# Kernel tuning notes

Measured on AMD Instinct MI355X. Metric: run time of the kernel, lower is better.

Reference implementation:

```python
import jax, jax.numpy as jnp
import numpy as np

UNITS = 1024
FEATURES = 16
OUT_STEPS = 24
LEAK = 0.001
MASK_VALUE = -1.0


def _plstm_step(h, c, x, kernel, rec_kernel, bias, period, phase, ratio_on):
    # Keras LSTMCell: gates ordered i, f, g, o
    z = x @ kernel + h @ rec_kernel + bias  # [B, 4U]
    i, f, g, o = jnp.split(z, 4, axis=-1)
    i = jax.nn.sigmoid(i)
    f = jax.nn.sigmoid(f)
    o = jax.nn.sigmoid(o)
    new_c = f * c + i * jnp.tanh(g)
    new_h = o * jnp.tanh(new_c)
    # phased time gate: time is the first feature channel
    t = x[:, :1]  # [B,1]
    cr = jnp.mod(t - phase, period) / period  # [B,U], floor-mod like tf %
    k_up = 2.0 * cr / ratio_on
    k = jnp.where(cr < ratio_on, 2.0 - k_up, LEAK * cr)
    k = jnp.where(cr < 0.5 * ratio_on, k_up, k)
    h_out = k * new_h + (1.0 - k) * h
    c_out = k * new_c + (1.0 - k) * c
    return h_out, c_out


def _dense_stack(h, w1, b1, w2, b2, w3, b3, wo, bo):
    h = jnp.tanh(h @ w1 + b1)
    h = jnp.tanh(h @ w2 + b2)
    h = jnp.tanh(h @ w3 + b3)
    return h @ wo + bo


def setup_inputs() -> dict:
    key = jax.random.key(0)
    ks = jax.random.split(key, 16)
    U, F = UNITS, FEATURES
    s = 1.0 / np.sqrt(U)
    x = jax.random.normal(ks[0], (256, 512, F), dtype=jnp.float32)
    kernel = jax.random.normal(ks[1], (F, 4 * U), dtype=jnp.float32) * (1.0 / np.sqrt(F))
    rec_kernel = jax.random.normal(ks[2], (U, 4 * U), dtype=jnp.float32) * s
    bias = jnp.zeros((4 * U,), dtype=jnp.float32)
    log_p = jax.random.uniform(ks[3], (U,), minval=jnp.log(1.0), maxval=jnp.log(100.0))
    period = jnp.exp(log_p).astype(jnp.float32)
    phase = (jax.random.uniform(ks[4], (U,)) * period).astype(jnp.float32)
    ratio_on = jnp.full((U,), 0.1, dtype=jnp.float32)
    w1 = jax.random.normal(ks[5], (U, U // 4), dtype=jnp.float32) * s
    b1 = jnp.zeros((U // 4,), dtype=jnp.float32)
    w2 = jax.random.normal(ks[6], (U // 4, U // 8), dtype=jnp.float32) * (1.0 / np.sqrt(U // 4))
    b2 = jnp.zeros((U // 8,), dtype=jnp.float32)
    w3 = jax.random.normal(ks[7], (U // 8, U // 16), dtype=jnp.float32) * (1.0 / np.sqrt(U // 8))
    b3 = jnp.zeros((U // 16,), dtype=jnp.float32)
    wo = jax.random.normal(ks[8], (U // 16, F), dtype=jnp.float32) * (1.0 / np.sqrt(U // 16))
    bo = jnp.zeros((F,), dtype=jnp.float32)
    return dict(x=x, kernel=kernel, rec_kernel=rec_kernel, bias=bias,
                period=period, phase=phase, ratio_on=ratio_on,
                w1=w1, b1=b1, w2=w2, b2=b2, w3=w3, b3=b3, wo=wo, bo=bo)


def reference(x, kernel, rec_kernel, bias, period, phase, ratio_on,
              w1, b1, w2, b2, w3, b3, wo, bo):
    B = x.shape[0]
    U = rec_kernel.shape[0]
    h0 = jnp.zeros((B, U), dtype=x.dtype)
    c0 = jnp.zeros((B, U), dtype=x.dtype)

    # warmup RNN over the input sequence (Masking(-1.0): skip all -1 steps)
    def warm_step(carry, xt):
        h, c = carry
        mask = jnp.any(xt != MASK_VALUE, axis=-1, keepdims=True)  # [B,1]
        hn, cn = _plstm_step(h, c, xt, kernel, rec_kernel, bias, period, phase, ratio_on)
        h = jnp.where(mask, hn, h)
        c = jnp.where(mask, cn, c)
        return (h, c), None

    (h, c), _ = jax.lax.scan(warm_step, (h0, c0), jnp.swapaxes(x, 0, 1))

    pred0 = _dense_stack(h, w1, b1, w2, b2, w3, b3, wo, bo)  # [B,F]

    def ar_step(carry, _):
        h, c, p = carry
        h, c = _plstm_step(h, c, p, kernel, rec_kernel, bias, period, phase, ratio_on)
        p = _dense_stack(h, w1, b1, w2, b2, w3, b3, wo, bo)
        return (h, c, p), p

    _, preds = jax.lax.scan(ar_step, (h, c, pred0), None, length=OUT_STEPS - 1)
    preds = jnp.concatenate([pred0[None], preds], axis=0)  # [S,B,F]
    return jnp.transpose(preds, (1, 0, 2))  # [B, out_steps, F]
```

## Files before the change

### kernel.cpp

```cpp
#include <hip/hip_runtime.h>
#include <hip/hip_bf16.h>

#define UNITS 1024
#define FEAT  16
#define TSTEPS 512
#define OUTSTEPS 24
#define BATCH 256
#define KTOT  1088
#define NROWS 4096

#define MPB   32
#define RPB   128
#define BSB   2320
#define HST2_OFF 74240
#define SMEM_BYTES 83968

#define NGBAR   96
#define CTR_TOT ((TSTEPS * 8 + NGBAR) * 16)

typedef __bf16 bf16x8 __attribute__((ext_vector_type(8)));
typedef float  f32x4  __attribute__((ext_vector_type(4)));

__device__ __forceinline__ float sigmoidf_(float x) { return 1.f / (1.f + __expf(-x)); }
__device__ __forceinline__ float tanhf_(float x)    { return 1.f - 2.f / (__expf(2.f * x) + 1.f); }

__global__ __launch_bounds__(256) void prep_weights(const float* __restrict__ kern,
                                                    const float* __restrict__ rec,
                                                    __bf16* __restrict__ Wcat) {
    __shared__ __align__(16) __bf16 tile[64][72];
    int r0 = blockIdx.x * 64;
    int k0 = blockIdx.y * 64;
    int t  = threadIdx.x;
    int c_off = t & 63;
    int k_grp = t >> 6;
    int g = c_off >> 4, ui = c_off & 15;
    int u0 = r0 >> 2;
    int c  = g * 1024 + u0 + ui;
    int rl = 4 * ui + g;
    for (int i = 0; i < 16; i++) {
        int k = k0 + k_grp * 16 + i;
        float v = 0.f;
        if (k < 16)        v = kern[(size_t)k * NROWS + c];
        else if (k < 1040) v = rec[(size_t)(k - 16) * NROWS + c];
        tile[rl][k_grp * 16 + i] = (__bf16)v;
    }
    __syncthreads();
    int rl2 = t >> 2, ch = t & 3;
    bf16x8* dst = (bf16x8*)(Wcat + (size_t)(r0 + rl2) * KTOT + k0 + ch * 16);
    const bf16x8* src = (const bf16x8*)&tile[rl2][ch * 16];
    dst[0] = src[0];
    dst[1] = src[1];
}

__global__ __launch_bounds__(256) void prep_state(const float* __restrict__ x,
                                                  __bf16* __restrict__ Ab0,
                                                  __bf16* __restrict__ Ab1,
                                                  float* __restrict__ hT,
                                                  unsigned int* __restrict__ ctr) {
    int tid = blockIdx.x * 256 + threadIdx.x;
    int np  = gridDim.x * 256;
    for (int i = tid; i < BATCH * UNITS; i += np) hT[i] = 0.f;
    const int AB = BATCH * KTOT;
    for (int i = tid; i < 2 * AB; i += np) {
        int which = (i < AB) ? 0 : 1;
        int p = i - which * AB;
        int col = p % KTOT;
        int m   = p / KTOT;
        __bf16 v = (__bf16)0.f;
        if (which == 0 && col < FEAT) v = (__bf16)x[(size_t)m * TSTEPS * FEAT + col];
        if (which == 0) Ab0[p] = v; else Ab1[p] = v;
    }
    for (int i = tid; i < CTR_TOT; i += np) ctr[i] = 0u;
}

__global__ __launch_bounds__(256) void prep_tv(const float* __restrict__ x,
                                               float* __restrict__ tvx,
                                               unsigned char* __restrict__ kflag,
                                               __bf16* __restrict__ xbf) {
    int m = blockIdx.x;
    for (int t = threadIdx.x; t < TSTEPS; t += 256) {
        const float* row = x + ((size_t)m * TSTEPS + t) * FEAT;
        f32x4 v0 = *(const f32x4*)row;
        f32x4 v1 = *(const f32x4*)(row + 4);
        f32x4 v2 = *(const f32x4*)(row + 8);
        f32x4 v3 = *(const f32x4*)(row + 12);
        bool keep = true;
#pragma unroll
        for (int i = 0; i < 4; ++i)
            keep = keep && (v0[i] == -1.f) && (v1[i] == -1.f) &&
                   (v2[i] == -1.f) && (v3[i] == -1.f);
        tvx[(size_t)t * BATCH + m]   = v0[0];
        kflag[(size_t)t * BATCH + m] = keep ? 1 : 0;
        __bf16* xo = xbf + ((size_t)t * BATCH + m) * 16;
        bf16x8 o0, o1;
#pragma unroll
        for (int i = 0; i < 4; ++i) { o0[i] = (__bf16)v0[i]; o0[4 + i] = (__bf16)v1[i]; }
#pragma unroll
        for (int i = 0; i < 4; ++i) { o1[i] = (__bf16)v2[i]; o1[4 + i] = (__bf16)v3[i]; }
        *(bf16x8*)xo = o0;
        *(bf16x8*)(xo + 8) = o1;
    }
}

__device__ __forceinline__ void gate_update(
    float z0, float z1, float z2, float z3,
    float bi, float bf, float bg, float bo,
    float ph, float rp, float ro, float k2,
    float tv, int kf, float& h, float& c) {
    float zi = z0 + bi, zf = z1 + bf, zg = z2 + bg, zo = z3 + bo;
    float ig = sigmoidf_(zi), fg = sigmoidf_(zf), og = sigmoidf_(zo);
    float gv = tanhf_(zg);
    float nc = fg * c + ig * gv;
    float nh = og * tanhf_(nc);
    float cr = (tv - ph) * rp;
    cr = cr - floorf(cr);
    float kup = cr * k2;
    float kk = (cr < ro) ? (2.f - kup) : (0.001f * cr);
    kk = (cr < 0.5f * ro) ? kup : kk;
    float ho = kk * nh + (1.f - kk) * h;
    float co = kk * nc + (1.f - kk) * c;
    if (kf) { ho = h; co = c; }
    h = ho; c = co;
}

#define BAR_SYNC(CP, COUNT) \
    __syncthreads(); \
    if (tid == 0) { \
        __hip_atomic_fetch_add((CP), 1u, __ATOMIC_RELAXED, __HIP_MEMORY_SCOPE_AGENT); \
        while (__hip_atomic_load((CP), __ATOMIC_RELAXED, __HIP_MEMORY_SCOPE_AGENT) < (COUNT)) \
            __builtin_amdgcn_s_sleep(2); \
    } \
    __syncthreads();

#define STEP2(ARP, AWP, TVBLOCK, DO_X) { \
    const char* src_ = (const char*)(ARP) + (size_t)(gm0 + (tid >> 4)) * (KTOT * 2) + (tid & 15) * 16; \
    char* dst_ = bsb + (tid >> 4) * BSB + (tid & 15) * 16; \
    f32x4 s0_; f32x4 s1_; f32x4 s2_; f32x4 s3_; f32x4 s4_; \
    f32x4 s5_; f32x4 s6_; f32x4 s7_; f32x4 s8_; \
    asm volatile( \
        "global_load_dwordx4 %0, %9, off sc0 sc1\n\t" \
        "global_load_dwordx4 %1, %9, off offset:256 sc0 sc1\n\t" \
        "global_load_dwordx4 %2, %9, off offset:512 sc0 sc1\n\t" \
        "global_load_dwordx4 %3, %9, off offset:768 sc0 sc1\n\t" \
        "global_load_dwordx4 %4, %9, off offset:1024 sc0 sc1\n\t" \
        "global_load_dwordx4 %5, %9, off offset:1280 sc0 sc1\n\t" \
        "global_load_dwordx4 %6, %9, off offset:1536 sc0 sc1\n\t" \
        "global_load_dwordx4 %7, %9, off offset:1792 sc0 sc1\n\t" \
        "global_load_dwordx4 %8, %9, off offset:2048 sc0 sc1" \
        : "=&v"(s0_), "=&v"(s1_), "=&v"(s2_), "=&v"(s3_), "=&v"(s4_), \
          "=&v"(s5_), "=&v"(s6_), "=&v"(s7_), "=&v"(s8_) \
        : "v"(src_) : "memory"); \
    float tv0f; float tv1f; int kf0; int kf1; \
    TVBLOCK \
    asm volatile("s_waitcnt vmcnt(0)" ::: "memory"); \
    __builtin_amdgcn_sched_barrier(0); \
    *(f32x4*)(dst_)        = s0_; \
    *(f32x4*)(dst_ + 256)  = s1_; \
    *(f32x4*)(dst_ + 512)  = s2_; \
    *(f32x4*)(dst_ + 768)  = s3_; \
    *(f32x4*)(dst_ + 1024) = s4_; \
    *(f32x4*)(dst_ + 1280) = s5_; \
    *(f32x4*)(dst_ + 1536) = s6_; \
    *(f32x4*)(dst_ + 1792) = s7_; \
    *(f32x4*)(dst_ + 2048) = s8_; \
    __syncthreads(); \
    f32x4 acc0 = {}; f32x4 acc1 = {}; \
    _Pragma("unroll") \
    for (int kt_ = 0; kt_ < 34; ++kt_) { \
        bf16x8 b0_ = *(const bf16x8*)(lbs + kt_ * 64); \
        bf16x8 b1_ = *(const bf16x8*)(lbs2 + kt_ * 64); \
        acc0 = __builtin_amdgcn_mfma_f32_16x16x32_bf16(areg[kt_], b0_, acc0, 0, 0, 0); \
        acc1 = __builtin_amdgcn_mfma_f32_16x16x32_bf16(areg[kt_], b1_, acc1, 0, 0, 0); \
    } \
    gate_update(acc0[0], acc0[1], acc0[2], acc0[3], Bi, Bf, Bg, Bo, Ph, Rp, Ro, K2, tv0f, kf0, h0, c0); \
    *(__bf16*)(hstageb + l16 * 64 + ucol2) = (__bf16)h0; \
    gate_update(acc1[0], acc1[1], acc1[2], acc1[3], Bi, Bf, Bg, Bo, Ph, Rp, Ro, K2, tv1f, kf1, h1, c1); \
    *(__bf16*)(hstageb + (16 + l16) * 64 + ucol2) = (__bf16)h1; \
    __syncthreads(); \
    if (tid < 256) { \
        int rw_ = tid >> 3; int ch_ = tid & 7; \
        unsigned long long v_ = *(const unsigned long long*)(hstageb + rw_ * 64 + ch_ * 8); \
        __hip_atomic_store((unsigned long long*)&(AWP)[(size_t)(gm0 + rw_) * KTOT + 16 + u0 + ch_ * 4], \
                           v_, __ATOMIC_RELAXED, __HIP_MEMORY_SCOPE_AGENT); \
    } \
    DO_X \
}

__global__ __launch_bounds__(512, 2) void rnn_all(
    const __bf16* __restrict__ Wcat,
    __bf16* __restrict__ Ab0, __bf16* __restrict__ Ab1,
    float* __restrict__ hT, float* __restrict__ a1T,
    const float* __restrict__ bias, const float* __restrict__ period,
    const float* __restrict__ phase, const float* __restrict__ ratio,
    const float* __restrict__ tvx, const unsigned char* __restrict__ kflag,
    const __bf16* __restrict__ xbf,
    const float* __restrict__ w1, const float* __restrict__ b1,
    const float* __restrict__ w2, const float* __restrict__ b2,
    const float* __restrict__ w3, const float* __restrict__ b3,
    const float* __restrict__ wo, const float* __restrict__ bo,
    float* __restrict__ out, unsigned int* ctr) {
    extern __shared__ __align__(16) char smem[];
    char*   bsb     = smem;
    char*   hstageb = smem + HST2_OFF;
    float*  redf    = (float*)smem;

    int b   = blockIdx.x;
    int mg  = b & 7, rbk = b >> 3;
    int tid = threadIdx.x;
    int wave = tid >> 6, lane = tid & 63;
    int l16 = lane & 15, quad = lane >> 4;
    int gm0 = mg * MPB;
    int r0  = rbk * RPB;
    int u0  = rbk * 32;

    bf16x8 areg[34];
    {
        const __bf16* wrow = Wcat + (size_t)(r0 + wave * 16 + l16) * KTOT + quad * 8;
#pragma unroll
        for (int kt = 0; kt < 34; ++kt) areg[kt] = *(const bf16x8*)(wrow + kt * 32);
    }

    int uu = u0 + wave * 4 + quad;
    int ucol2 = (wave * 4 + quad) * 2;
    float Bi = bias[uu], Bf = bias[UNITS + uu];
    float Bg = bias[2 * UNITS + uu], Bo = bias[3 * UNITS + uu];
    float Ph = phase[uu];
    float Rp = 1.f / period[uu];
    float Ro = ratio[uu], K2 = 2.f / Ro;
    float h0 = 0.f, c0 = 0.f, h1 = 0.f, c1 = 0.f;

    const char* lbs  = bsb + l16 * BSB + quad * 16;
    const char* lbs2 = lbs + 16 * BSB;
    unsigned int* gctr = ctr + TSTEPS * 8 * 16;

#pragma unroll 1
    for (int t = 0; t < TSTEPS; ++t) {
        const __bf16* Ar = (t & 1) ? Ab1 : Ab0;
        __bf16*       Aw = (t & 1) ? Ab0 : Ab1;
        STEP2(Ar, Aw,
            { tv0f = tvx[(size_t)t * BATCH + gm0 + l16];
              tv1f = tvx[(size_t)t * BATCH + gm0 + 16 + l16];
              kf0  = kflag[(size_t)t * BATCH + gm0 + l16];
              kf1  = kflag[(size_t)t * BATCH + gm0 + 16 + l16]; },
            else if (rbk == 0 && t + 1 < TSTEPS) {
                int i_ = tid - 256; int row_ = i_ >> 3; int ch_ = i_ & 7;
                unsigned v_ = *(const unsigned*)
                    &xbf[((size_t)(t + 1) * BATCH + gm0 + row_) * 16 + ch_ * 2];
                __hip_atomic_store((unsigned*)&Aw[(size_t)(gm0 + row_) * KTOT + ch_ * 2],
                                   v_, __ATOMIC_RELAXED, __HIP_MEMORY_SCOPE_AGENT);
            })
        if (t + 1 < TSTEPS) {
            unsigned int* cp_ = ctr + ((size_t)t * 8 + mg) * 16;
            BAR_SYNC(cp_, 32u)
        }
    }

    int gb2 = b & 3, rb2 = b >> 2;
    int gm2 = gb2 * 64;
    int par = 0;
    int gi = 0;
#pragma unroll 1
    for (int s = 0; s < OUTSTEPS; ++s) {
        __hip_atomic_store(&hT[(size_t)uu * BATCH + gm0 + l16], h0,
                           __ATOMIC_RELAXED, __HIP_MEMORY_SCOPE_AGENT);
        __hip_atomic_store(&hT[(size_t)uu * BATCH + gm0 + 16 + l16], h1,
                           __ATOMIC_RELAXED, __HIP_MEMORY_SCOPE_AGENT);
        { unsigned int* cp_ = gctr + (size_t)gi * 16; gi++; BAR_SYNC(cp_, 256u) }

        {
            const float* hp0 = hT + (size_t)(wave * 128) * BATCH + gm2 + lane;
            const float* hp1 = hp0 + 4 * BATCH;
            const float* wp0 = w1 + (size_t)(wave * 128) * 256 + rb2 * 4;
            const float* wp1 = wp0 + 4 * 256;
            float d0 = 0.f, d1 = 0.f, d2 = 0.f, d3 = 0.f;
#pragma unroll 1
            for (int it = 0; it < 16; ++it) {
                float x0, x1, x2, x3, x4, x5, x6, x7;
                f32x4 w0_, w1_, w2_, w3_, w4_, w5_, w6_, w7_;
                asm volatile(
                    "global_load_dword %0, %16, off sc0 sc1\n\t"
                    "global_load_dword %1, %16, off offset:1024 sc0 sc1\n\t"
                    "global_load_dword %2, %16, off offset:2048 sc0 sc1\n\t"
                    "global_load_dword %3, %16, off offset:3072 sc0 sc1\n\t"
                    "global_load_dword %4, %17, off sc0 sc1\n\t"
                    "global_load_dword %5, %17, off offset:1024 sc0 sc1\n\t"
                    "global_load_dword %6, %17, off offset:2048 sc0 sc1\n\t"
                    "global_load_dword %7, %17, off offset:3072 sc0 sc1\n\t"
                    "global_load_dwordx4 %8, %18, off\n\t"
                    "global_load_dwordx4 %9, %18, off offset:1024\n\t"
                    "global_load_dwordx4 %10, %18, off offset:2048\n\t"
                    "global_load_dwordx4 %11, %18, off offset:3072\n\t"
                    "global_load_dwordx4 %12, %19, off\n\t"
                    "global_load_dwordx4 %13, %19, off offset:1024\n\t"
                    "global_load_dwordx4 %14, %19, off offset:2048\n\t"
                    "global_load_dwordx4 %15, %19, off offset:3072"
                    : "=&v"(x0), "=&v"(x1), "=&v"(x2), "=&v"(x3),
                      "=&v"(x4), "=&v"(x5), "=&v"(x6), "=&v"(x7),
                      "=&v"(w0_), "=&v"(w1_), "=&v"(w2_), "=&v"(w3_),
                      "=&v"(w4_), "=&v"(w5_), "=&v"(w6_), "=&v"(w7_)
                    : "v"(hp0), "v"(hp1), "v"(wp0), "v"(wp1)
                    : "memory");
                asm volatile("s_waitcnt vmcnt(0)" ::: "memory");
                __builtin_amdgcn_sched_barrier(0);
                d0 += x0 * w0_[0]; d1 += x0 * w0_[1]; d2 += x0 * w0_[2]; d3 += x0 * w0_[3];
                d0 += x1 * w1_[0]; d1 += x1 * w1_[1]; d2 += x1 * w1_[2]; d3 += x1 * w1_[3];
                d0 += x2 * w2_[0]; d1 += x2 * w2_[1]; d2 += x2 * w2_[2]; d3 += x2 * w2_[3];
                d0 += x3 * w3_[0]; d1 += x3 * w3_[1]; d2 += x3 * w3_[2]; d3 += x3 * w3_[3];
                d0 += x4 * w4_[0]; d1 += x4 * w4_[1]; d2 += x4 * w4_[2]; d3 += x4 * w4_[3];
                d0 += x5 * w5_[0]; d1 += x5 * w5_[1]; d2 += x5 * w5_[2]; d3 += x5 * w5_[3];
                d0 += x6 * w6_[0]; d1 += x6 * w6_[1]; d2 += x6 * w6_[2]; d3 += x6 * w6_[3];
                d0 += x7 * w7_[0]; d1 += x7 * w7_[1]; d2 += x7 * w7_[2]; d3 += x7 * w7_[3];
                hp0 += 8 * BATCH; hp1 += 8 * BATCH;
                wp0 += 8 * 256;   wp1 += 8 * 256;
            }
            redf[wave * 256 + 0 * 64 + lane] = d0;
            redf[wave * 256 + 1 * 64 + lane] = d1;
            redf[wave * 256 + 2 * 64 + lane] = d2;
            redf[wave * 256 + 3 * 64 + lane] = d3;
            __syncthreads();
            if (tid < 256) {
                int q = tid >> 6, ml2 = tid & 63;
                float sum = 0.f;
#pragma unroll
                for (int w = 0; w < 8; ++w) sum += redf[w * 256 + q * 64 + ml2];
                sum = tanhf_(sum + b1[rb2 * 4 + q]);
                __hip_atomic_store(&a1T[(size_t)(rb2 * 4 + q) * 256 + gm2 + ml2], sum,
                                   __ATOMIC_RELAXED, __HIP_MEMORY_SCOPE_AGENT);
            }
        }
        { unsigned int* cp_ = gctr + (size_t)gi * 16; gi++; BAR_SYNC(cp_, 256u) }

        if (rb2 < 8) {
            int m0t = gm2 + rb2 * 8;
            float* a1s = (float*)smem;
            float* a2s = a1s + 8 * 256;
            float* a3s = a2s + 8 * 128;
            {
                float v0, v1, v2, v3;
                int i0 = tid, i1 = tid + 512, i2 = tid + 1024, i3 = tid + 1536;
                const float* p0 = a1T + (size_t)(i0 >> 3) * 256 + m0t + (i0 & 7);
                const float* p1 = a1T + (size_t)(i1 >> 3) * 256 + m0t + (i1 & 7);
                const float* p2 = a1T + (size_t)(i2 >> 3) * 256 + m0t + (i2 & 7);
                const float* p3 = a1T + (size_t)(i3 >> 3) * 256 + m0t + (i3 & 7);
                asm volatile(
                    "global_load_dword %0, %4, off sc0 sc1\n\t"
                    "global_load_dword %1, %5, off sc0 sc1\n\t"
                    "global_load_dword %2, %6, off sc0 sc1\n\t"
                    "global_load_dword %3, %7, off sc0 sc1"
                    : "=&v"(v0), "=&v"(v1), "=&v"(v2), "=&v"(v3)
                    : "v"(p0), "v"(p1), "v"(p2), "v"(p3) : "memory");
                asm volatile("s_waitcnt vmcnt(0)" ::: "memory");
                __builtin_amdgcn_sched_barrier(0);
                a1s[(i0 & 7) * 256 + (i0 >> 3)] = v0;
                a1s[(i1 & 7) * 256 + (i1 >> 3)] = v1;
                a1s[(i2 & 7) * 256 + (i2 >> 3)] = v2;
                a1s[(i3 & 7) * 256 + (i3 >> 3)] = v3;
            }
            __syncthreads();
            if (tid < 256) {
                int j = tid & 127, r2 = tid >> 7;
                float acc[4] = {0.f, 0.f, 0.f, 0.f};
                for (int k = 0; k < 256; k++) {
                    float w = w2[(size_t)k * 128 + j];
#pragma unroll
                    for (int q = 0; q < 4; q++) acc[q] += a1s[(r2 * 4 + q) * 256 + k] * w;
                }
                float bb = b2[j];
#pragma unroll
                for (int q = 0; q < 4; q++) a2s[(r2 * 4 + q) * 128 + j] = tanhf_(acc[q] + bb);
            }
            __syncthreads();
            if (tid < 256) {
                int j = tid & 63, r2 = tid >> 6;
                float acc[2] = {0.f, 0.f};
                for (int k = 0; k < 128; k++) {
                    float w = w3[(size_t)k * 64 + j];
#pragma unroll
                    for (int q = 0; q < 2; q++) acc[q] += a2s[(r2 * 2 + q) * 128 + k] * w;
                }
                float bb = b3[j];
#pragma unroll
                for (int q = 0; q < 2; q++) a3s[(r2 * 2 + q) * 64 + j] = tanhf_(acc[q] + bb);
            }
            __syncthreads();
            if (tid < 128) {
                int j = tid & 15, r = tid >> 4;
                float accv = 0.f;
                for (int k = 0; k < 64; k++) accv += a3s[r * 64 + k] * wo[(size_t)k * 16 + j];
                float v = accv + bo[j];
                __hip_atomic_store(&out[(size_t)(m0t + r) * (OUTSTEPS * FEAT) + s * FEAT + j],
                                   v, __ATOMIC_RELAXED, __HIP_MEMORY_SCOPE_AGENT);
                a1s[r * 16 + j] = v;
            }
            __syncthreads();
            if (tid < 64) {
                int r = tid >> 3, jp = tid & 7;
                __bf16 lo = (__bf16)a1s[r * 16 + jp * 2];
                __bf16 hi = (__bf16)a1s[r * 16 + jp * 2 + 1];
                unsigned int pv = (unsigned int)(*(unsigned short*)&lo) |
                                  ((unsigned int)(*(unsigned short*)&hi) << 16);
                __bf16* xdst = (par ? Ab1 : Ab0) + (size_t)(m0t + r) * KTOT + jp * 2;
                __hip_atomic_store((unsigned int*)xdst, pv,
                                   __ATOMIC_RELAXED, __HIP_MEMORY_SCOPE_AGENT);
            }
        }
        { unsigned int* cp_ = gctr + (size_t)gi * 16; gi++; BAR_SYNC(cp_, 256u) }

        if (s < OUTSTEPS - 1) {
            const __bf16* Ar = par ? Ab1 : Ab0;
            __bf16*       Aw = par ? Ab0 : Ab1;
            STEP2(Ar, Aw,
                { const float* p0_ = out + (size_t)(gm0 + l16) * (OUTSTEPS * FEAT) + s * FEAT;
                  const float* p1_ = p0_ + (size_t)16 * (OUTSTEPS * FEAT);
                  asm volatile(
                      "global_load_dword %0, %2, off sc0 sc1\n\t"
                      "global_load_dword %1, %3, off sc0 sc1"
                      : "=&v"(tv0f), "=&v"(tv1f) : "v"(p0_), "v"(p1_) : "memory");
                  kf0 = 0; kf1 = 0; },
                )
            par ^= 1;
        }
    }
}

extern "C" void kernel_launch(void* const* d_in, const int* in_sizes, int n_in,
                              void* d_out, int out_size, void* d_ws, size_t ws_size,
                              hipStream_t stream) {
    (void)in_sizes; (void)n_in; (void)out_size; (void)ws_size;
    const float* x      = (const float*)d_in[0];
    const float* kern   = (const float*)d_in[1];
    const float* rec    = (const float*)d_in[2];
    const float* bias   = (const float*)d_in[3];
    const float* period = (const float*)d_in[4];
    const float* phase  = (const float*)d_in[5];
    const float* ratio  = (const float*)d_in[6];
    const float* w1 = (const float*)d_in[7];
    const float* b1 = (const float*)d_in[8];
    const float* w2 = (const float*)d_in[9];
    const float* b2 = (const float*)d_in[10];
    const float* w3 = (const float*)d_in[11];
    const float* b3 = (const float*)d_in[12];
    const float* wo = (const float*)d_in[13];
    const float* bo = (const float*)d_in[14];
    float* out = (float*)d_out;

    char* ws = (char*)d_ws;
    const size_t WCAT_B = (size_t)NROWS * KTOT * 2;
    const size_t AB_B   = (size_t)BATCH * KTOT * 2;
    __bf16* Wcat = (__bf16*)ws;
    __bf16* Ab0  = (__bf16*)(ws + WCAT_B);
    __bf16* Ab1  = (__bf16*)(ws + WCAT_B + AB_B);
    float*  hT   = (float*)(ws + WCAT_B + 2 * AB_B);
    float*  a1T  = hT + (size_t)BATCH * UNITS;
    float*  tvx  = a1T + (size_t)BATCH * 256;
    __bf16* xbf  = (__bf16*)(tvx + (size_t)TSTEPS * BATCH);
    unsigned char* kflag = (unsigned char*)(xbf + (size_t)TSTEPS * BATCH * 16);
    unsigned int*  ctr   = (unsigned int*)(kflag + (size_t)TSTEPS * BATCH);

    (void)hipFuncSetAttribute((const void*)rnn_all,
                              hipFuncAttributeMaxDynamicSharedMemorySize,
                              (int)SMEM_BYTES);

    prep_weights<<<dim3(64, 17), 256, 0, stream>>>(kern, rec, Wcat);
    prep_state<<<512, 256, 0, stream>>>(x, Ab0, Ab1, hT, ctr);
    prep_tv<<<256, 256, 0, stream>>>(x, tvx, kflag, xbf);

    rnn_all<<<dim3(256), dim3(512), SMEM_BYTES, stream>>>(
        Wcat, Ab0, Ab1, hT, a1T, bias, period, phase, ratio,
        tvx, kflag, xbf, w1, b1, w2, b2, w3, b3, wo, bo, out, ctr);
}
```

Before: 4.297 ms.

## Split K dimension across wave halves with LDS reduction in recurrent GEMM

Each wave now computes a 2x2 block of MFMA tiles (two row tiles by two batch tiles) over half of the K dimension instead of one row tile over the full K. The two K-halves exchange partial sums through a new LDS reduction buffer, and each wave then applies the gate update for one batch half. The intent is to halve the serial MFMA dependency chain per step and reuse each B fragment across two A tiles, which shortens per-timestep latency on the critical recurrent path. The cost is an extra LDS write/read, an additional __syncthreads per step, and more shared memory.

```diff
diff --git a/kernel.cpp b/kernel.cpp
--- a/kernel.cpp
+++ b/kernel.cpp
@@ -12,8 +12,9 @@
 #define MPB   32
 #define RPB   128
 #define BSB   2320
-#define HST2_OFF 74240
-#define SMEM_BYTES 83968
+#define RED2_OFF 74240
+#define HST2_OFF (RED2_OFF + 16384)
+#define SMEM_BYTES (HST2_OFF + 2048)
 
 #define NGBAR   96
 #define CTR_TOT ((TSTEPS * 8 + NGBAR) * 16)
@@ -164,18 +165,36 @@
     *(f32x4*)(dst_ + 1792) = s7_; \
     *(f32x4*)(dst_ + 2048) = s8_; \
     __syncthreads(); \
-    f32x4 acc0 = {}; f32x4 acc1 = {}; \
+    f32x4 acc00 = {}; f32x4 acc01 = {}; f32x4 acc10 = {}; f32x4 acc11 = {}; \
     _Pragma("unroll") \
-    for (int kt_ = 0; kt_ < 34; ++kt_) { \
+    for (int kt_ = 0; kt_ < 17; ++kt_) { \
         bf16x8 b0_ = *(const bf16x8*)(lbs + kt_ * 64); \
         bf16x8 b1_ = *(const bf16x8*)(lbs2 + kt_ * 64); \
-        acc0 = __builtin_amdgcn_mfma_f32_16x16x32_bf16(areg[kt_], b0_, acc0, 0, 0, 0); \
-        acc1 = __builtin_amdgcn_mfma_f32_16x16x32_bf16(areg[kt_], b1_, acc1, 0, 0, 0); \
+        acc00 = __builtin_amdgcn_mfma_f32_16x16x32_bf16(areg0[kt_], b0_, acc00, 0, 0, 0); \
+        acc01 = __builtin_amdgcn_mfma_f32_16x16x32_bf16(areg0[kt_], b1_, acc01, 0, 0, 0); \
+        acc10 = __builtin_amdgcn_mfma_f32_16x16x32_bf16(areg1[kt_], b0_, acc10, 0, 0, 0); \
+        acc11 = __builtin_amdgcn_mfma_f32_16x16x32_bf16(areg1[kt_], b1_, acc11, 0, 0, 0); \
     } \
-    gate_update(acc0[0], acc0[1], acc0[2], acc0[3], Bi, Bf, Bg, Bo, Ph, Rp, Ro, K2, tv0f, kf0, h0, c0); \
-    *(__bf16*)(hstageb + l16 * 64 + ucol2) = (__bf16)h0; \
-    gate_update(acc1[0], acc1[1], acc1[2], acc1[3], Bi, Bf, Bg, Bo, Ph, Rp, Ro, K2, tv1f, kf1, h1, c1); \
-    *(__bf16*)(hstageb + (16 + l16) * 64 + ucol2) = (__bf16)h1; \
+     \
+    { \
+        int po_ = (rq * 4 + (kh ^ 1) * 2) * 64 + lane; \
+        redv[po_]      = kh ? acc00 : acc01; \
+        redv[po_ + 64] = kh ? acc10 : acc11; \
+    } \
+    __syncthreads(); \
+    { \
+        int so_ = (rq * 4 + kh * 2) * 64 + lane; \
+        f32x4 zA_ = (kh ? acc01 : acc00) + redv[so_]; \
+        f32x4 zB_ = (kh ? acc11 : acc10) + redv[so_ + 64]; \
+        float tvf = kh ? tv1f : tv0f; \
+        int kf = kh ? kf1 : kf0; \
+        gate_update(zA_[0], zA_[1], zA_[2], zA_[3], BiA, BfA, BgA, BoA, \
+                    PhA, RpA, RoA, K2A, tvf, kf, hA, cA); \
+        *(__bf16*)(hstageb + mloc * 64 + ucolA) = (__bf16)hA; \
+        gate_update(zB_[0], zB_[1], zB_[2], zB_[3], BiB, BfB, BgB, BoB, \
+                    PhB, RpB, RoB, K2B, tvf, kf, hB, cB); \
+        *(__bf16*)(hstageb + mloc * 64 + ucolB) = (__bf16)hB; \
+    } \
     __syncthreads(); \
     if (tid < 256) { \
         int rw_ = tid >> 3; int ch_ = tid & 7; \
@@ -201,6 +220,7 @@
     float* __restrict__ out, unsigned int* ctr) {
     extern __shared__ __align__(16) char smem[];
     char*   bsb     = smem;
+    f32x4*  redv    = (f32x4*)(smem + RED2_OFF);
     char*   hstageb = smem + HST2_OFF;
     float*  redf    = (float*)smem;
 
@@ -208,28 +228,40 @@
     int mg  = b & 7, rbk = b >> 3;
     int tid = threadIdx.x;
     int wave = tid >> 6, lane = tid & 63;
+    int rq = wave & 3, kh = wave >> 2;
     int l16 = lane & 15, quad = lane >> 4;
     int gm0 = mg * MPB;
     int r0  = rbk * RPB;
     int u0  = rbk * 32;
 
-    bf16x8 areg[34];
+    bf16x8 areg0[17], areg1[17];
     {
-        const __bf16* wrow = Wcat + (size_t)(r0 + wave * 16 + l16) * KTOT + quad * 8;
-#pragma unroll
-        for (int kt = 0; kt < 34; ++kt) areg[kt] = *(const bf16x8*)(wrow + kt * 32);
+        const __bf16* wr0 = Wcat + (size_t)(r0 + rq * 32 + l16) * KTOT + kh * 544 + quad * 8;
+        const __bf16* wr1 = wr0 + (size_t)16 * KTOT;
+#pragma unroll
+        for (int kt = 0; kt < 17; ++kt) {
+            areg0[kt] = *(const bf16x8*)(wr0 + kt * 32);
+            areg1[kt] = *(const bf16x8*)(wr1 + kt * 32);
+        }
     }
 
-    int uu = u0 + wave * 4 + quad;
-    int ucol2 = (wave * 4 + quad) * 2;
-    float Bi = bias[uu], Bf = bias[UNITS + uu];
-    float Bg = bias[2 * UNITS + uu], Bo = bias[3 * UNITS + uu];
-    float Ph = phase[uu];
-    float Rp = 1.f / period[uu];
-    float Ro = ratio[uu], K2 = 2.f / Ro;
-    float h0 = 0.f, c0 = 0.f, h1 = 0.f, c1 = 0.f;
-
-    const char* lbs  = bsb + l16 * BSB + quad * 16;
+    int uuA = u0 + rq * 8 + quad;
+    int uuB = uuA + 4;
+    int mloc = kh * 16 + l16;
+    int mm = gm0 + mloc;
+    int ucolA = (rq * 8 + quad) * 2;
+    int ucolB = ucolA + 8;
+    float BiA = bias[uuA],             BiB = bias[uuB];
+    float BfA = bias[UNITS + uuA],     BfB = bias[UNITS + uuB];
+    float BgA = bias[2 * UNITS + uuA], BgB = bias[2 * UNITS + uuB];
+    float BoA = bias[3 * UNITS + uuA], BoB = bias[3 * UNITS + uuB];
+    float PhA = phase[uuA], PhB = phase[uuB];
+    float RpA = 1.f / period[uuA], RpB = 1.f / period[uuB];
+    float RoA = ratio[uuA], RoB = ratio[uuB];
+    float K2A = 2.f / RoA,  K2B = 2.f / RoB;
+    float hA = 0.f, cA = 0.f, hB = 0.f, cB = 0.f;
+
+    const char* lbs  = bsb + l16 * BSB + kh * 1088 + quad * 16;
     const char* lbs2 = lbs + 16 * BSB;
     unsigned int* gctr = ctr + TSTEPS * 8 * 16;
 
@@ -261,9 +293,9 @@
     int gi = 0;
 #pragma unroll 1
     for (int s = 0; s < OUTSTEPS; ++s) {
-        __hip_atomic_store(&hT[(size_t)uu * BATCH + gm0 + l16], h0,
+        __hip_atomic_store(&hT[(size_t)uuA * BATCH + mm], hA,
                            __ATOMIC_RELAXED, __HIP_MEMORY_SCOPE_AGENT);
-        __hip_atomic_store(&hT[(size_t)uu * BATCH + gm0 + 16 + l16], h1,
+        __hip_atomic_store(&hT[(size_t)uuB * BATCH + mm], hB,
                            __ATOMIC_RELAXED, __HIP_MEMORY_SCOPE_AGENT);
         { unsigned int* cp_ = gctr + (size_t)gi * 16; gi++; BAR_SYNC(cp_, 256u) }
 
```

New measurement: 4.150 ms. -3.4%, faster.
